# Performance work log

Measured on AMD Instinct MI355X. Metric: run time of the kernel, lower is better.

## Reference

```python
import math
import jax, jax.numpy as jnp
import numpy as np

THETA = 2.0 ** 16
TWO_PI = 2.0 * math.pi


def _freqs(N):
    # quantize(arange(N), 2) = floor(t/2)*2 -> paired frequencies
    idx = jnp.floor(jnp.arange(N, dtype=jnp.float32) / 2.0) * 2.0
    return 1.0 / (THETA ** (idx / N)) / TWO_PI  # (N,)


def _rope(v, cos, sin):
    # rotate pairs: (-v_odd, v_even) interleaved back to original layout
    v_rot = jnp.stack((-v[..., 1::2], v[..., ::2]), axis=-1).reshape(v.shape)
    return v * cos + v_rot * sin


def setup_inputs() -> dict:
    key = jax.random.key(0)
    k1, k2 = jax.random.split(key)
    B, nh, T, N, D = 1, 4, 2048, 8192, 256
    Q = jax.random.normal(k1, (B, nh, T, N), dtype=jnp.float32) * 0.02
    V = jax.random.normal(k2, (B, 1, T, D), dtype=jnp.float32)
    return {"Q": Q, "V": V}


def reference(Q, V):
    # Q: (B, nh, T, N) sparse neuron space; V: (B, 1, T, D) embedding space; K is Q
    T, N = Q.shape[2], Q.shape[3]
    freqs = _freqs(N)
    phases = jnp.arange(T, dtype=jnp.float32)[:, None] * freqs[None, :]  # (T, N)
    ang = (phases % 1.0) * TWO_PI
    cos, sin = jnp.cos(ang), jnp.sin(ang)
    QR = _rope(Q, cos, sin)  # (B, nh, T, N)
    scores = jnp.einsum('bhtn,bhsn->bhts', QR, QR)  # (B, nh, T, T)
    causal = jnp.tril(jnp.ones((T, T), dtype=bool), k=-1)  # strictly lower
    scores = jnp.where(causal, scores, 0.0)
    # V broadcasts over heads: (B, nh, T, T) @ (B, 1, T, D) -> (B, nh, T, D)
    return jnp.matmul(scores, V)
```

## Files before the change

kernel.cpp:

```cpp
#include <hip/hip_runtime.h>

#define LDS_AS __attribute__((address_space(3)))
#define GLB_AS __attribute__((address_space(1)))

typedef __attribute__((ext_vector_type(8))) short bf16x8;
typedef __attribute__((ext_vector_type(4))) float f32x4;
typedef __attribute__((ext_vector_type(16))) float f32x16;

static constexpr int NH = 4;
static constexpr int T  = 2048;
static constexpr int N  = 8192;
static constexpr int D  = 256;

__device__ inline unsigned short f2bf(float f) {
    unsigned int u = __float_as_uint(f);
    u += 0x7FFFu + ((u >> 16) & 1u);
    return (unsigned short)(u >> 16);
}

__device__ inline void gl2lds16(const void* g, void* l) {
    __builtin_amdgcn_global_load_lds((GLB_AS void*)g, (LDS_AS void*)l, 16, 0, 0);
}

__global__ void rope_kernel(const float* __restrict__ Q, unsigned short* __restrict__ QR) {
    int g = blockIdx.x * 256 + threadIdx.x;
    int base = g << 2;
    int n = base & (N - 1);
    int t = (base >> 13) & (T - 1);
    const float4 q = *(const float4*)(Q + (size_t)base);
    float tf = (float)t;
    const float inv2pi = 0.15915494309189535f;
    float f0 = exp2f((float)n       * (-1.0f / 512.0f)) * inv2pi;
    float f1 = exp2f((float)(n + 2) * (-1.0f / 512.0f)) * inv2pi;
    float r0 = tf * f0; r0 -= floorf(r0);
    float r1 = tf * f1; r1 -= floorf(r1);
    float s0 = __builtin_amdgcn_sinf(r0), c0 = __builtin_amdgcn_cosf(r0);
    float s1 = __builtin_amdgcn_sinf(r1), c1 = __builtin_amdgcn_cosf(r1);
    ushort4 o;
    o.x = f2bf(q.x * c0 - q.y * s0);
    o.y = f2bf(q.y * c0 + q.x * s0);
    o.z = f2bf(q.z * c1 - q.w * s1);
    o.w = f2bf(q.w * c1 + q.z * s1);
    *(ushort4*)(QR + (size_t)base) = o;
}

__global__ void vt_kernel(const float* __restrict__ V, unsigned short* __restrict__ Vt) {
    __shared__ unsigned short tile[64 * 65];
    int tb = blockIdx.x >> 2, db = blockIdx.x & 3;
    int t0 = tb * 64, d0 = db * 64;
    int tid = threadIdx.x;
    #pragma unroll
    for (int r = 0; r < 16; r++) {
        int idx = tid + r * 256;
        int tl = idx >> 6, dl = idx & 63;
        tile[tl * 65 + dl] = f2bf(V[(size_t)(t0 + tl) * D + d0 + dl]);
    }
    __syncthreads();
    #pragma unroll
    for (int r = 0; r < 16; r++) {
        int idx = tid + r * 256;
        int dl = idx >> 6, tl = idx & 63;
        Vt[(size_t)(d0 + dl) * T + t0 + tl] = tile[tl * 65 + dl];
    }
}

__global__ __launch_bounds__(256, 2) void gemm1_kernel(const unsigned short* __restrict__ QR,
                                                       unsigned short* __restrict__ S, int KS) {
    __shared__ __align__(16) unsigned short As[3][4096];
    __shared__ __align__(16) unsigned short Bs[3][8192];

    int bx = blockIdx.x;
    int per_h = 72 * KS;
    int h = bx / per_h;
    int rem = bx % per_h;
    int task = rem / KS;
    int ksp = rem % KS;
    int bi = 0, cum = 0;
    for (; bi < 16; bi++) { int nb = (bi >> 1) + 1; if (cum + nb > task) break; cum += nb; }
    int bj = task - cum;

    const unsigned short* A = QR + (size_t)h * T * N + (size_t)bi * 128 * N;
    const unsigned short* B = QR + (size_t)h * T * N + (size_t)bj * 256 * N;

    int KN = N / KS;
    int k_begin = ksp * KN;
    int nit = KN / 32;

    int tid = threadIdx.x;
    int lane = tid & 63, wave = tid >> 6;
    int wm = wave >> 1, wn = wave & 1;

    int srow = tid >> 2;
    int q = tid & 3;
    int scol_sw = (q ^ ((srow >> 1) & 3)) * 8;
    const unsigned short* Asrc = A + (size_t)srow * N + scol_sw;
    const unsigned short* Bsrc = B + (size_t)srow * N + scol_sw;

    f32x16 acc[2][4];
    #pragma unroll
    for (int i = 0; i < 2; i++)
        #pragma unroll
        for (int j = 0; j < 4; j++)
            #pragma unroll
            for (int r = 0; r < 16; r++) acc[i][j][r] = 0.0f;

    #pragma unroll
    for (int p = 0; p < 2; p++) {
        int k0 = k_begin + p * 32;
        gl2lds16(Asrc + k0,                   &As[p][tid * 8]);
        gl2lds16(Asrc + (size_t)64 * N + k0,  &As[p][2048 + tid * 8]);
        gl2lds16(Bsrc + k0,                   &Bs[p][tid * 8]);
        gl2lds16(Bsrc + (size_t)64 * N + k0,  &Bs[p][2048 + tid * 8]);
        gl2lds16(Bsrc + (size_t)128 * N + k0, &Bs[p][4096 + tid * 8]);
        gl2lds16(Bsrc + (size_t)192 * N + k0, &Bs[p][6144 + tid * 8]);
    }

    int l31 = lane & 31, hi = lane >> 5, fl = (lane >> 1) & 3;

    int cur = 0, nxt2 = 2;
    for (int it = 0; it < nit; it++) {
        if (it + 1 < nit) {
            asm volatile("s_waitcnt vmcnt(6)" ::: "memory");
        } else {
            asm volatile("s_waitcnt vmcnt(0)" ::: "memory");
        }
        __builtin_amdgcn_s_barrier();
        __builtin_amdgcn_sched_barrier(0);

        bf16x8 a2[2][2], b2[4][2];
        #pragma unroll
        for (int i = 0; i < 2; i++)
            #pragma unroll
            for (int kk = 0; kk < 2; kk++)
                a2[i][kk] = *(const bf16x8*)&As[cur][(wm * 64 + i * 32 + l31) * 32
                                                     + ((kk * 2 + hi) ^ fl) * 8];
        #pragma unroll
        for (int j = 0; j < 4; j++)
            #pragma unroll
            for (int kk = 0; kk < 2; kk++)
                b2[j][kk] = *(const bf16x8*)&Bs[cur][(wn * 128 + j * 32 + l31) * 32
                                                     + ((kk * 2 + hi) ^ fl) * 8];

        if (it + 2 < nit) {
            int k0 = k_begin + (it + 2) * 32;
            gl2lds16(Asrc + k0,                   &As[nxt2][tid * 8]);
            gl2lds16(Asrc + (size_t)64 * N + k0,  &As[nxt2][2048 + tid * 8]);
            gl2lds16(Bsrc + k0,                   &Bs[nxt2][tid * 8]);
            gl2lds16(Bsrc + (size_t)64 * N + k0,  &Bs[nxt2][2048 + tid * 8]);
            gl2lds16(Bsrc + (size_t)128 * N + k0, &Bs[nxt2][4096 + tid * 8]);
            gl2lds16(Bsrc + (size_t)192 * N + k0, &Bs[nxt2][6144 + tid * 8]);
        }

        __builtin_amdgcn_s_setprio(1);
        #pragma unroll
        for (int kk = 0; kk < 2; kk++)
            #pragma unroll
            for (int j = 0; j < 4; j++)
                #pragma unroll
                for (int i = 0; i < 2; i++)
                    acc[i][j] = __builtin_amdgcn_mfma_f32_32x32x16_bf16(a2[i][kk], b2[j][kk],
                                                                        acc[i][j], 0, 0, 0);
        __builtin_amdgcn_s_setprio(0);

        cur  = (cur  == 2) ? 0 : cur  + 1;
        nxt2 = (nxt2 == 2) ? 0 : nxt2 + 1;
    }

    unsigned short* Sh = S + (size_t)ksp * NH * T * T + (size_t)h * T * T;
    int col = lane & 31;
    int rbase = (lane >> 5) * 4;
    #pragma unroll
    for (int i = 0; i < 2; i++) {
        #pragma unroll
        for (int j = 0; j < 4; j++) {
            int s_g = bj * 256 + wn * 128 + j * 32 + col;
            #pragma unroll
            for (int reg = 0; reg < 16; reg++) {
                int t_g = bi * 128 + wm * 64 + i * 32 + (reg & 3) + 8 * (reg >> 2) + rbase;
                float v = (s_g < t_g) ? acc[i][j][reg] : 0.0f;
                Sh[(size_t)t_g * T + s_g] = f2bf(v);
            }
        }
    }
}

__global__ __launch_bounds__(256, 2) void gemm2_kernel(const unsigned short* __restrict__ S,
                                                       const unsigned short* __restrict__ Vt,
                                                       float* __restrict__ out, int KS) {
    __shared__ __align__(16) unsigned short As[3][4096];
    __shared__ __align__(16) unsigned short Bs[3][4096];

    int bx = blockIdx.x;
    int per_h = 2 * 72;
    int h = bx / per_h;
    int rem = bx % per_h;
    int dblk = rem / 72;
    int tc = rem % 72;
    int bi = 0, cum = 0;
    for (; bi < 16; bi++) { int nc = (bi + 2) >> 1; if (cum + nc > tc) break; cum += nc; }
    int c = tc - cum;

    int kend = (bi + 1) * 128;
    int cstart = c * 256;
    int clen = min(256, kend - cstart);
    int cpk = clen >> 5;
    int ls = (KS == 4) ? 2 : (KS == 2) ? 1 : 0;
    int nit = cpk << ls;

    const unsigned short* Sh = S + (size_t)h * T * T + (size_t)bi * 128 * T + cstart;
    const size_t sstride = (size_t)NH * T * T;
    const unsigned short* B = Vt + (size_t)dblk * 128 * T + cstart;

    int tid = threadIdx.x;
    int lane = tid & 63, wave = tid >> 6;
    int wm = wave >> 1, wn = wave & 1;
    int quad = lane >> 4, l16 = lane & 15;

    int srow = tid >> 2;
    int q = tid & 3;
    int scol_sw = (q ^ ((srow >> 1) & 3)) * 8;

    f32x4 acc[4][4];
    #pragma unroll
    for (int i = 0; i < 4; i++)
        #pragma unroll
        for (int j = 0; j < 4; j++)
            #pragma unroll
            for (int r = 0; r < 4; r++) acc[i][j][r] = 0.0f;

    #pragma unroll
    for (int p = 0; p < 2; p++) {
        int ks0 = p & (KS - 1);
        int k00 = (p >> ls) * 32;
        const unsigned short* An = Sh + (size_t)ks0 * sstride + k00;
        const unsigned short* Bn = B + k00;
        gl2lds16(An + (size_t)srow * T + scol_sw,        &As[p][tid * 8]);
        gl2lds16(An + (size_t)(srow + 64) * T + scol_sw, &As[p][2048 + tid * 8]);
        gl2lds16(Bn + (size_t)srow * T + scol_sw,        &Bs[p][tid * 8]);
        gl2lds16(Bn + (size_t)(srow + 64) * T + scol_sw, &Bs[p][2048 + tid * 8]);
    }

    int fl16 = (l16 >> 1) & 3;
    int cur = 0, nxt2 = 2;
    for (int i = 0; i < nit; i++) {
        if (i + 1 < nit) {
            asm volatile("s_waitcnt vmcnt(4)" ::: "memory");
        } else {
            asm volatile("s_waitcnt vmcnt(0)" ::: "memory");
        }
        __builtin_amdgcn_s_barrier();
        __builtin_amdgcn_sched_barrier(0);

        bf16x8 a[4], b[4];
        #pragma unroll
        for (int ii = 0; ii < 4; ii++) {
            a[ii] = *(const bf16x8*)&As[cur][(wm * 64 + ii * 16 + l16) * 32 + (quad ^ fl16) * 8];
            b[ii] = *(const bf16x8*)&Bs[cur][(wn * 64 + ii * 16 + l16) * 32 + (quad ^ fl16) * 8];
        }

        if (i + 2 < nit) {
            int ksn = (i + 2) & (KS - 1);
            int k0n = ((i + 2) >> ls) * 32;
            const unsigned short* An = Sh + (size_t)ksn * sstride + k0n;
            const unsigned short* Bn = B + k0n;
            gl2lds16(An + (size_t)srow * T + scol_sw,        &As[nxt2][tid * 8]);
            gl2lds16(An + (size_t)(srow + 64) * T + scol_sw, &As[nxt2][2048 + tid * 8]);
            gl2lds16(Bn + (size_t)srow * T + scol_sw,        &Bs[nxt2][tid * 8]);
            gl2lds16(Bn + (size_t)(srow + 64) * T + scol_sw, &Bs[nxt2][2048 + tid * 8]);
        }

        __builtin_amdgcn_s_setprio(1);
        #pragma unroll
        for (int ii = 0; ii < 4; ii++)
            #pragma unroll
            for (int j = 0; j < 4; j++)
                acc[ii][j] = __builtin_amdgcn_mfma_f32_16x16x32_bf16(a[ii], b[j], acc[ii][j], 0, 0, 0);
        __builtin_amdgcn_s_setprio(0);

        cur  = (cur  == 2) ? 0 : cur  + 1;
        nxt2 = (nxt2 == 2) ? 0 : nxt2 + 1;
    }

    float* oh = out + (size_t)h * T * D;
    #pragma unroll
    for (int i = 0; i < 4; i++) {
        int t_base = bi * 128 + wm * 64 + i * 16 + quad * 4;
        #pragma unroll
        for (int j = 0; j < 4; j++) {
            int d_g = dblk * 128 + wn * 64 + j * 16 + l16;
            #pragma unroll
            for (int r = 0; r < 4; r++) {
                int t_g = t_base + r;
                atomicAdd(&oh[(size_t)t_g * D + d_g], acc[i][j][r]);
            }
        }
    }
}

extern "C" void kernel_launch(void* const* d_in, const int* in_sizes, int n_in,
                              void* d_out, int out_size, void* d_ws, size_t ws_size,
                              hipStream_t stream) {
    const float* Q = (const float*)d_in[0];
    const float* V = (const float*)d_in[1];
    float* out = (float*)d_out;

    const size_t qr_elems = (size_t)NH * T * N;
    const size_t vt_elems = (size_t)D * T;
    const size_t s_elems  = (size_t)NH * T * T;

    int KS = 1;
    for (int cand : {4, 2, 1}) {
        if (ws_size >= (qr_elems + vt_elems + (size_t)cand * s_elems) * sizeof(unsigned short)) {
            KS = cand; break;
        }
    }
    if (ws_size < (qr_elems + vt_elems + (size_t)KS * s_elems) * sizeof(unsigned short)) return;

    unsigned short* QR = (unsigned short*)d_ws;
    unsigned short* Vt = QR + qr_elems;
    unsigned short* S  = Vt + vt_elems;

    rope_kernel<<<(NH * T * N / 4) / 256, 256, 0, stream>>>(Q, QR);
    vt_kernel<<<(T / 64) * (D / 64), 256, 0, stream>>>(V, Vt);
    gemm1_kernel<<<NH * 72 * KS, 256, 0, stream>>>(QR, S, KS);
    hipMemsetAsync(d_out, 0, (size_t)out_size * sizeof(float), stream);
    gemm2_kernel<<<NH * 2 * 72, 256, 0, stream>>>(S, Vt, out, KS);
}
```

Before: 588.9 us.

## Restructure gemm2 to full-K tiles with 32x32 MFMA and direct stores

gemm2 drops the split of the K dimension into 256-wide chunks. Each block now owns a 128x64 output tile and runs the whole causal K range itself, using 32x32x16 MFMA instead of 16x16x32. Results are written with plain stores, which removes the output memset and the atomicAdd traffic. In exchange, the grid shrinks to 256 blocks with K lengths that differ widely across blocks (up to 2048), so tail imbalance and lower parallelism are a risk. The narrower D tile also makes each block reread the S rows for every D block.

```diff
diff --git a/kernel.cpp b/kernel.cpp
--- a/kernel.cpp
+++ b/kernel.cpp
@@ -184,97 +184,92 @@
     }
 }
 
-__global__ __launch_bounds__(256, 2) void gemm2_kernel(const unsigned short* __restrict__ S,
+__global__ __launch_bounds__(256, 4) void gemm2_kernel(const unsigned short* __restrict__ S,
                                                        const unsigned short* __restrict__ Vt,
                                                        float* __restrict__ out, int KS) {
     __shared__ __align__(16) unsigned short As[3][4096];
-    __shared__ __align__(16) unsigned short Bs[3][4096];
+    __shared__ __align__(16) unsigned short Bs[3][2048];
 
     int bx = blockIdx.x;
-    int per_h = 2 * 72;
-    int h = bx / per_h;
-    int rem = bx % per_h;
-    int dblk = rem / 72;
-    int tc = rem % 72;
-    int bi = 0, cum = 0;
-    for (; bi < 16; bi++) { int nc = (bi + 2) >> 1; if (cum + nc > tc) break; cum += nc; }
-    int c = tc - cum;
+    int h = bx >> 6;
+    int rem = bx & 63;
+    int dblk = rem >> 4;
+    int bi = rem & 15;
 
     int kend = (bi + 1) * 128;
-    int cstart = c * 256;
-    int clen = min(256, kend - cstart);
-    int cpk = clen >> 5;
+    int nk = kend >> 5;
     int ls = (KS == 4) ? 2 : (KS == 2) ? 1 : 0;
-    int nit = cpk << ls;
-
-    const unsigned short* Sh = S + (size_t)h * T * T + (size_t)bi * 128 * T + cstart;
+    int nit = nk << ls;
+
+    const unsigned short* Sh = S + (size_t)h * T * T + (size_t)bi * 128 * T;
     const size_t sstride = (size_t)NH * T * T;
-    const unsigned short* B = Vt + (size_t)dblk * 128 * T + cstart;
+    const unsigned short* Bb = Vt + (size_t)dblk * 64 * T;
 
     int tid = threadIdx.x;
     int lane = tid & 63, wave = tid >> 6;
     int wm = wave >> 1, wn = wave & 1;
-    int quad = lane >> 4, l16 = lane & 15;
 
     int srow = tid >> 2;
     int q = tid & 3;
     int scol_sw = (q ^ ((srow >> 1) & 3)) * 8;
-
-    f32x4 acc[4][4];
-    #pragma unroll
-    for (int i = 0; i < 4; i++)
-        #pragma unroll
-        for (int j = 0; j < 4; j++)
-            #pragma unroll
-            for (int r = 0; r < 4; r++) acc[i][j][r] = 0.0f;
+    const unsigned short* Arow = Sh + (size_t)srow * T + scol_sw;
+    const unsigned short* Brow = Bb + (size_t)srow * T + scol_sw;
+
+    f32x16 acc[2];
+    #pragma unroll
+    for (int i = 0; i < 2; i++)
+        #pragma unroll
+        for (int r = 0; r < 16; r++) acc[i][r] = 0.0f;
 
     #pragma unroll
     for (int p = 0; p < 2; p++) {
-        int ks0 = p & (KS - 1);
-        int k00 = (p >> ls) * 32;
-        const unsigned short* An = Sh + (size_t)ks0 * sstride + k00;
-        const unsigned short* Bn = B + k00;
-        gl2lds16(An + (size_t)srow * T + scol_sw,        &As[p][tid * 8]);
-        gl2lds16(An + (size_t)(srow + 64) * T + scol_sw, &As[p][2048 + tid * 8]);
-        gl2lds16(Bn + (size_t)srow * T + scol_sw,        &Bs[p][tid * 8]);
-        gl2lds16(Bn + (size_t)(srow + 64) * T + scol_sw, &Bs[p][2048 + tid * 8]);
-    }
-
-    int fl16 = (l16 >> 1) & 3;
+        int ksp = p & (KS - 1);
+        int k0p = (p >> ls) * 32;
+        const unsigned short* An = Arow + (size_t)ksp * sstride + k0p;
+        gl2lds16(An,                     &As[p][tid * 8]);
+        gl2lds16(An + (size_t)64 * T,    &As[p][2048 + tid * 8]);
+        gl2lds16(Brow + k0p,             &Bs[p][tid * 8]);
+    }
+
+    int l31 = lane & 31, hi = lane >> 5, fl = (lane >> 1) & 3;
+
     int cur = 0, nxt2 = 2;
     for (int i = 0; i < nit; i++) {
         if (i + 1 < nit) {
-            asm volatile("s_waitcnt vmcnt(4)" ::: "memory");
+            asm volatile("s_waitcnt vmcnt(3)" ::: "memory");
         } else {
             asm volatile("s_waitcnt vmcnt(0)" ::: "memory");
         }
         __builtin_amdgcn_s_barrier();
         __builtin_amdgcn_sched_barrier(0);
 
-        bf16x8 a[4], b[4];
-        #pragma unroll
-        for (int ii = 0; ii < 4; ii++) {
-            a[ii] = *(const bf16x8*)&As[cur][(wm * 64 + ii * 16 + l16) * 32 + (quad ^ fl16) * 8];
-            b[ii] = *(const bf16x8*)&Bs[cur][(wn * 64 + ii * 16 + l16) * 32 + (quad ^ fl16) * 8];
-        }
+        bf16x8 a2[2][2], b2[2];
+        #pragma unroll
+        for (int i2 = 0; i2 < 2; i2++)
+            #pragma unroll
+            for (int kk = 0; kk < 2; kk++)
+                a2[i2][kk] = *(const bf16x8*)&As[cur][(wm * 64 + i2 * 32 + l31) * 32
+                                                      + ((kk * 2 + hi) ^ fl) * 8];
+        #pragma unroll
+        for (int kk = 0; kk < 2; kk++)
+            b2[kk] = *(const bf16x8*)&Bs[cur][(wn * 32 + l31) * 32 + ((kk * 2 + hi) ^ fl) * 8];
 
         if (i + 2 < nit) {
             int ksn = (i + 2) & (KS - 1);
             int k0n = ((i + 2) >> ls) * 32;
-            const unsigned short* An = Sh + (size_t)ksn * sstride + k0n;
-            const unsigned short* Bn = B + k0n;
-            gl2lds16(An + (size_t)srow * T + scol_sw,        &As[nxt2][tid * 8]);
-            gl2lds16(An + (size_t)(srow + 64) * T + scol_sw, &As[nxt2][2048 + tid * 8]);
-            gl2lds16(Bn + (size_t)srow * T + scol_sw,        &Bs[nxt2][tid * 8]);
-            gl2lds16(Bn + (size_t)(srow + 64) * T + scol_sw, &Bs[nxt2][2048 + tid * 8]);
+            const unsigned short* An = Arow + (size_t)ksn * sstride + k0n;
+            gl2lds16(An,                  &As[nxt2][tid * 8]);
+            gl2lds16(An + (size_t)64 * T, &As[nxt2][2048 + tid * 8]);
+            gl2lds16(Brow + k0n,          &Bs[nxt2][tid * 8]);
         }
 
         __builtin_amdgcn_s_setprio(1);
         #pragma unroll
-        for (int ii = 0; ii < 4; ii++)
-            #pragma unroll
-            for (int j = 0; j < 4; j++)
-                acc[ii][j] = __builtin_amdgcn_mfma_f32_16x16x32_bf16(a[ii], b[j], acc[ii][j], 0, 0, 0);
+        for (int kk = 0; kk < 2; kk++)
+            #pragma unroll
+            for (int i2 = 0; i2 < 2; i2++)
+                acc[i2] = __builtin_amdgcn_mfma_f32_32x32x16_bf16(a2[i2][kk], b2[kk],
+                                                                  acc[i2], 0, 0, 0);
         __builtin_amdgcn_s_setprio(0);
 
         cur  = (cur  == 2) ? 0 : cur  + 1;
@@ -282,17 +277,15 @@
     }
 
     float* oh = out + (size_t)h * T * D;
-    #pragma unroll
-    for (int i = 0; i < 4; i++) {
-        int t_base = bi * 128 + wm * 64 + i * 16 + quad * 4;
-        #pragma unroll
-        for (int j = 0; j < 4; j++) {
-            int d_g = dblk * 128 + wn * 64 + j * 16 + l16;
-            #pragma unroll
-            for (int r = 0; r < 4; r++) {
-                int t_g = t_base + r;
-                atomicAdd(&oh[(size_t)t_g * D + d_g], acc[i][j][r]);
-            }
+    int col = lane & 31;
+    int rbase = (lane >> 5) * 4;
+    int d_g = dblk * 64 + wn * 32 + col;
+    #pragma unroll
+    for (int i2 = 0; i2 < 2; i2++) {
+        #pragma unroll
+        for (int reg = 0; reg < 16; reg++) {
+            int t_g = bi * 128 + wm * 64 + i2 * 32 + (reg & 3) + 8 * (reg >> 2) + rbase;
+            oh[(size_t)t_g * D + d_g] = acc[i2][reg];
         }
     }
 }
@@ -323,6 +316,5 @@
     rope_kernel<<<(NH * T * N / 4) / 256, 256, 0, stream>>>(Q, QR);
     vt_kernel<<<(T / 64) * (D / 64), 256, 0, stream>>>(V, Vt);
     gemm1_kernel<<<NH * 72 * KS, 256, 0, stream>>>(QR, S, KS);
-    hipMemsetAsync(d_out, 0, (size_t)out_size * sizeof(float), stream);
-    gemm2_kernel<<<NH * 2 * 72, 256, 0, stream>>>(S, Vt, out, KS);
-}
+    gemm2_kernel<<<NH * 16 * 4, 256, 0, stream>>>(S, Vt, out, KS);
+}
```

After: 624.8 us. +6.1%, slower.
